# Kernel tuning notes

Measured on AMD Instinct MI355X. Metric: run time of the kernel, lower is better.

The kernel has to match this reference:

```python
import jax, jax.numpy as jnp
import numpy as np

DIM = 1024
S_SIZE = 512
M_SIZE = 4096
L_SIZE = 8192
MERGE_THRESHOLD = 0.98
L_ALPHA = 0.1
K_PROMOTE = max(1, S_SIZE // 4)  # torch: min(len(candidates), max(1, s_size//4)); candidates >> s_size here


def _l2norm(x, axis=-1):
    # F.normalize(p=2) with eps clamp
    return x / jnp.maximum(jnp.linalg.norm(x, axis=axis, keepdims=True), 1e-12)


def _update(processed_tokens, s_memory, m_memory, l_memory, m_utility, l_utility, wq, bq, wk, bk, s_ptr):
    cand = processed_tokens.reshape(-1, DIM)
    # --- S tier: scatter top-k-norm candidates into ring buffer (vectorized; K<=S so slots distinct) ---
    norms = jnp.linalg.norm(cand, axis=1)
    _, top_idx = jax.lax.top_k(norms, K_PROMOTE)
    pos = (s_ptr + jnp.arange(K_PROMOTE)) % S_SIZE
    s_mem = s_memory.at[pos].set(cand[top_idx])
    s_ptr_new = (s_ptr + K_PROMOTE) % S_SIZE
    # --- promotion attention (1 head, only attn weights used): pick best short-term slot ---
    q = l_memory.mean(axis=0) @ wq.T + bq                      # [dim]
    kproj = s_mem @ wk.T + bk                                  # [S, dim]
    attn = jax.nn.softmax(kproj @ q / jnp.sqrt(jnp.asarray(DIM, cand.dtype)))
    best_s_idx = jnp.argmax(attn)
    candidate = s_mem[best_s_idx]                              # [dim]

    # --- M tier: promote / merge / replace ---
    def not_full(mm, mu):
        ridx = jnp.argmin(mu)
        return mm.at[ridx].set(candidate), mu.at[ridx].set(mu.mean() + 1e-5)

    def full(mm, mu):
        mm_norm = _l2norm(mm)
        sims = mm_norm @ _l2norm(candidate)                    # [M]
        msi = jnp.argmax(sims)
        sim_cand = sims[msi]

        def merge_with_candidate(mm, mu):
            merged = _l2norm((mm[msi] + candidate) / 2.0)
            return mm.at[msi].set(merged), mu.at[msi].set((mu[msi] + mu.mean()) / 2.0)

        def try_internal_merge(mm, mu):
            # most redundant pair: strict lower triangle of cosine sim matrix
            sim_mat = mm_norm @ mm_norm.T                      # [M, M]
            sim_mat = jnp.where(jnp.triu(jnp.ones((M_SIZE, M_SIZE), bool)), -1.0, sim_mat)
            flat = jnp.argmax(sim_mat)
            internal_sim = sim_mat.reshape(-1)[flat]
            idx1, idx2 = flat // M_SIZE, flat % M_SIZE

            def do_pair_merge(mm, mu):
                merged = _l2norm((mm[idx1] + mm[idx2]) / 2.0)
                mm2 = mm.at[idx1].set(merged).at[idx2].set(candidate)
                mu1 = mu.at[idx1].set((mu[idx1] + mu[idx2]) / 2.0)
                mu2 = mu1.at[idx2].set(mu1.mean() + 1e-5)      # torch recomputes mean after idx1 write
                return mm2, mu2

            def replace_weakest(mm, mu):
                li = jnp.argmin(mu)
                stronger = jnp.linalg.norm(candidate) > jnp.linalg.norm(mm[li])
                mm2 = jnp.where(stronger, mm.at[li].set(candidate), mm)
                mu2 = jnp.where(stronger, mu.at[li].set(mu.mean() + 1e-5), mu)
                return mm2, mu2

            return jax.lax.cond(internal_sim > MERGE_THRESHOLD, do_pair_merge, replace_weakest, mm, mu)

        return jax.lax.cond(sim_cand > MERGE_THRESHOLD, merge_with_candidate, try_internal_merge, mm, mu)

    is_m_full = ~jnp.any(m_utility == 0)
    m_mem, m_util = jax.lax.cond(is_m_full, full, not_full, m_memory, m_utility)
    # --- L tier: consolidate most-used M slot into least-used L slot ---
    mi = jnp.argmax(m_util)
    lj = jnp.argmin(l_utility)
    consolidated = (1.0 - L_ALPHA) * l_memory[lj] + L_ALPHA * m_mem[mi]
    l_mem = l_memory.at[lj].set(consolidated)
    l_util = l_utility.at[lj].set(l_utility.mean())            # mean of pre-write values
    return s_mem, m_mem, l_mem, m_util, l_util, s_ptr_new


def setup_inputs() -> dict:
    key = jax.random.key(0)
    ks = jax.random.split(key, 10)
    scale = 1.0 / np.sqrt(DIM)
    return {
        "processed_tokens": jax.random.normal(ks[0], (4, 4096, DIM), jnp.float32),
        "s_memory": jax.random.normal(ks[1], (S_SIZE, DIM), jnp.float32),
        "m_memory": jax.random.normal(ks[2], (M_SIZE, DIM), jnp.float32),
        "l_memory": jax.random.normal(ks[3], (L_SIZE, DIM), jnp.float32),
        "m_utility": jax.random.uniform(ks[4], (M_SIZE,), jnp.float32) + 0.01,  # >0 -> 'm full' branch
        "l_utility": jax.random.uniform(ks[5], (L_SIZE,), jnp.float32) + 0.01,
        "wq": jax.random.normal(ks[6], (DIM, DIM), jnp.float32) * scale,
        "bq": jnp.zeros((DIM,), jnp.float32),
        "wk": jax.random.normal(ks[7], (DIM, DIM), jnp.float32) * scale,
        "bk": jnp.zeros((DIM,), jnp.float32),
        "s_ptr": 0,
    }


def reference(processed_tokens, s_memory, m_memory, l_memory, m_utility, l_utility, wq, bq, wk, bk, s_ptr):
    return _update(processed_tokens, s_memory, m_memory, l_memory, m_utility, l_utility, wq, bq, wk, bk, s_ptr)
```

## Files before the change

kernel.cpp:

```cpp
#include <hip/hip_runtime.h>

#define DIMV 1024
#define SSZ 512
#define MSZ 4096
#define LSZ 8192
#define KPROM 128
#define NCAND 16384
#define NPAIR 528

typedef __attribute__((ext_vector_type(4))) float f32x4;
typedef __attribute__((ext_vector_type(4))) unsigned int u32x4;
typedef __attribute__((ext_vector_type(4))) unsigned short u16x4;
typedef __attribute__((ext_vector_type(8))) __bf16 bf16x8;

#define OUT_S 0ull
#define OUT_M 524288ull
#define OUT_L 4718592ull
#define OUT_MU 13107200ull
#define OUT_LU 13111296ull
#define OUT_SPTR 13119488ull

#define SC_BF16 0ull
#define SC_NORMS 2100000ull
#define SC_TOPIDX 2117000ull
#define SC_LPART 2120000ull
#define SC_RV 2260000ull
#define SC_LMEAN 2262000ull
#define SC_LOGITS 2413000ull
#define SC_BEST 2414000ull
#define SC_MNORM 2415000ull
#define SC_SIMS 2420000ull
#define SC_PPV 2425000ull
#define SC_PPI 2427000ull

__device__ __forceinline__ float wave_sum(float v) {
#pragma unroll
  for (int o = 32; o > 0; o >>= 1) v += __shfl_down(v, o, 64);
  return v;
}
__device__ __forceinline__ void wave_maxidx(float& v, int& i) {
#pragma unroll
  for (int o = 32; o > 0; o >>= 1) {
    float ov = __shfl_down(v, o, 64);
    int oi = __shfl_down(i, o, 64);
    if (ov > v || (ov == v && oi < i)) { v = ov; i = oi; }
  }
}
__device__ __forceinline__ void wave_minidx(float& v, int& i) {
#pragma unroll
  for (int o = 32; o > 0; o >>= 1) {
    float ov = __shfl_down(v, o, 64);
    int oi = __shfl_down(i, o, 64);
    if (ov < v || (ov == v && oi < i)) { v = ov; i = oi; }
  }
}
__device__ __forceinline__ unsigned short f2bf(float x) {
  unsigned u = __float_as_uint(x);
  return (unsigned short)((u + 0x7FFFu + ((u >> 16) & 1u)) >> 16);
}
__device__ __forceinline__ void gload16(const unsigned short* g, unsigned short* l) {
  __builtin_amdgcn_global_load_lds((const __attribute__((address_space(1))) unsigned int*)(g),
                                   (__attribute__((address_space(3))) unsigned int*)(l), 16, 0, 0);
}

__global__ void kA(const float* __restrict__ cand, const float* __restrict__ l_memory,
                   const float* __restrict__ m, float* __restrict__ norms,
                   float* __restrict__ lpart, unsigned short* __restrict__ mb,
                   float* __restrict__ mnorm, float* __restrict__ rv) {
  int b = blockIdx.x, t = threadIdx.x, lane = t & 63, w = t >> 6;
  if (b < 128) {
    if (b == 0) {
      f32x4 z = {0.f, 0.f, 0.f, 0.f};
      ((f32x4*)rv)[t] = z;
    }
    f32x4 a0 = {0.f, 0.f, 0.f, 0.f}, a1 = a0, a2 = a0, a3 = a0;
    const f32x4* base = (const f32x4*)(l_memory + (size_t)b * 64 * DIMV);
#pragma unroll 4
    for (int r = 0; r < 64; r += 4) {
      a0 += base[(r + 0) * 256 + t];
      a1 += base[(r + 1) * 256 + t];
      a2 += base[(r + 2) * 256 + t];
      a3 += base[(r + 3) * 256 + t];
    }
    f32x4 a = (a0 + a1) + (a2 + a3);
    ((f32x4*)(lpart + (size_t)b * DIMV))[t] = a;
  } else if (b < 1152) {
    int r0 = (b - 128) * 16 + w * 4;
    const f32x4* base4 = (const f32x4*)(cand + (size_t)r0 * DIMV);
    float s0 = 0.f, s1 = 0.f, s2 = 0.f, s3 = 0.f;
#pragma unroll
    for (int k = 0; k < 16; ++k) {
      f32x4 v = base4[k * 64 + lane];
      float d = v.x * v.x + v.y * v.y + v.z * v.z + v.w * v.w;
      if (k < 4) s0 += d;
      else if (k < 8) s1 += d;
      else if (k < 12) s2 += d;
      else s3 += d;
    }
    f32x4 sv = {s0, s1, s2, s3};
#pragma unroll
    for (int o = 32; o > 0; o >>= 1) {
      sv.x += __shfl_down(sv.x, o, 64);
      sv.y += __shfl_down(sv.y, o, 64);
      sv.z += __shfl_down(sv.z, o, 64);
      sv.w += __shfl_down(sv.w, o, 64);
    }
    if (lane == 0) {
      f32x4 o4 = {sqrtf(sv.x), sqrtf(sv.y), sqrtf(sv.z), sqrtf(sv.w)};
      *((f32x4*)(norms + r0)) = o4;
    }
  } else {
    int r0 = (b - 1152) * 16 + w * 4;
    const f32x4* base4 = (const f32x4*)(m + (size_t)r0 * DIMV);
    u16x4* mb4 = (u16x4*)(mb + (size_t)r0 * DIMV);
    float s0 = 0.f, s1 = 0.f, s2 = 0.f, s3 = 0.f;
#pragma unroll
    for (int k = 0; k < 16; ++k) {
      int i = k * 64 + lane;
      f32x4 v = base4[i];
      float d = v.x * v.x + v.y * v.y + v.z * v.z + v.w * v.w;
      if (k < 4) s0 += d;
      else if (k < 8) s1 += d;
      else if (k < 12) s2 += d;
      else s3 += d;
      u16x4 h;
      h.x = f2bf(v.x); h.y = f2bf(v.y); h.z = f2bf(v.z); h.w = f2bf(v.w);
      mb4[i] = h;
    }
    f32x4 sv = {s0, s1, s2, s3};
#pragma unroll
    for (int o = 32; o > 0; o >>= 1) {
      sv.x += __shfl_down(sv.x, o, 64);
      sv.y += __shfl_down(sv.y, o, 64);
      sv.z += __shfl_down(sv.z, o, 64);
      sv.w += __shfl_down(sv.w, o, 64);
    }
    if (lane == 0) {
      f32x4 o4 = {sqrtf(sv.x), sqrtf(sv.y), sqrtf(sv.z), sqrtf(sv.w)};
      *((f32x4*)(mnorm + r0)) = o4;
    }
  }
}

__device__ int scan_excl_1024(int v, int* sh, int* total) {
  int t = threadIdx.x;
  sh[t] = v;
  __syncthreads();
  for (int o = 1; o < 1024; o <<= 1) {
    int x = (t >= o) ? sh[t - o] : 0;
    __syncthreads();
    sh[t] += x;
    __syncthreads();
  }
  int incl = sh[t];
  *total = sh[1023];
  __syncthreads();
  return incl - v;
}

__global__ void kT(const float* __restrict__ norms, int* __restrict__ topidx,
                   const float* __restrict__ lpart, float* __restrict__ lmean) {
  int t = threadIdx.x;
  if (blockIdx.x == 1) {
    float s0 = 0.f, s1 = 0.f, s2 = 0.f, s3 = 0.f;
    for (int p = 0; p < 128; p += 4) {
      s0 += lpart[(size_t)(p + 0) * DIMV + t];
      s1 += lpart[(size_t)(p + 1) * DIMV + t];
      s2 += lpart[(size_t)(p + 2) * DIMV + t];
      s3 += lpart[(size_t)(p + 3) * DIMV + t];
    }
    lmean[t] = ((s0 + s1) + (s2 + s3)) * (1.f / 8192.f);
    return;
  }
  int w = t >> 6;
  __shared__ int sh[1024];
  __shared__ int histW[16][256];
  __shared__ unsigned s_selkey[KPROM];
  __shared__ int s_selidx[KPROM];
  __shared__ int s_digit, s_sub;
  unsigned key[16];
#pragma unroll
  for (int j = 0; j < 16; ++j) key[j] = __float_as_uint(norms[t * 16 + j]);

  unsigned prefix = 0, himask = 0;
  int remaining = KPROM;
  for (int p = 24; p >= 0; p -= 8) {
#pragma unroll
    for (int i = 0; i < 4; ++i) ((int*)histW)[t + i * 1024] = 0;
    __syncthreads();
#pragma unroll
    for (int j = 0; j < 16; ++j)
      if ((key[j] & himask) == prefix) atomicAdd(&histW[w][(key[j] >> p) & 255], 1);
    __syncthreads();
    if (t < 256) {
      int h = 0;
#pragma unroll
      for (int w2 = 0; w2 < 16; ++w2) h += histW[w2][t];
      sh[t] = h;
    }
    __syncthreads();
    for (int o = 1; o < 256; o <<= 1) {
      int x = (t < 256 && t + o < 256) ? sh[t + o] : 0;
      __syncthreads();
      if (t < 256) sh[t] += x;
      __syncthreads();
    }
    if (t < 256) {
      int sfex = (t < 255) ? sh[t + 1] : 0;
      if (sfex < remaining && remaining <= sh[t]) { s_digit = t; s_sub = sfex; }
    }
    __syncthreads();
    prefix |= ((unsigned)s_digit) << p;
    remaining -= s_sub;
    himask |= (0xFFu << p);
    __syncthreads();
  }
  unsigned T = prefix;

  int cgt = 0, ceq = 0;
#pragma unroll
  for (int j = 0; j < 16; ++j) { cgt += (key[j] > T); ceq += (key[j] == T); }
  int total_gt, total_eq;
  int sgt = scan_excl_1024(cgt, sh, &total_gt);
  int seq = scan_excl_1024(ceq, sh, &total_eq);
  int need_eq = KPROM - total_gt;
  int g = sgt, e = seq;
#pragma unroll
  for (int j = 0; j < 16; ++j) {
    if (key[j] > T) { s_selkey[g] = key[j]; s_selidx[g] = t * 16 + j; ++g; }
    else if (key[j] == T) {
      if (e < need_eq) { s_selkey[total_gt + e] = key[j]; s_selidx[total_gt + e] = t * 16 + j; }
      ++e;
    }
  }
  __syncthreads();
  if (t < KPROM) {
    unsigned mk = s_selkey[t];
    int mi = s_selidx[t];
    int rank = 0;
    for (int q2 = 0; q2 < KPROM; ++q2) {
      unsigned qk = s_selkey[q2];
      int qi = s_selidx[q2];
      rank += (qk > mk || (qk == mk && qi < mi)) ? 1 : 0;
    }
    topidx[rank] = mi;
  }
}

__global__ void kBC(const float* __restrict__ cand, const float* __restrict__ s_memory,
                    const int* __restrict__ topidx, const int* __restrict__ s_ptr,
                    const float* __restrict__ wq, const float* __restrict__ bq,
                    const float* __restrict__ wk, const float* __restrict__ lmean,
                    float* __restrict__ out_s, float* __restrict__ out_sptr,
                    float* __restrict__ rv) {
  int b = blockIdx.x, t = threadIdx.x, lane = t & 63, w = t >> 6;
  if (b < 512) {
    int sp = s_ptr[0];
    int k = (b - sp + SSZ) & (SSZ - 1);
    const float* src = (k < KPROM) ? (cand + (size_t)topidx[k] * DIMV) : (s_memory + (size_t)b * DIMV);
    ((f32x4*)(out_s + (size_t)b * DIMV))[t] = ((const f32x4*)src)[t];
    if (b == 0 && t == 0) out_sptr[0] = (float)((sp + KPROM) % SSZ);
    return;
  }
  __shared__ float qs[8];
  int qb = b - 512;
  const f32x4* lm = (const f32x4*)lmean;
#pragma unroll
  for (int rr = 0; rr < 2; ++rr) {
    int d = qb * 8 + w * 2 + rr;
    const f32x4* row = (const f32x4*)(wq + (size_t)d * DIMV);
    float s = 0.f;
#pragma unroll
    for (int c = 0; c < 4; ++c) {
      f32x4 a = row[c * 64 + lane], bb = lm[c * 64 + lane];
      s += a.x * bb.x + a.y * bb.y + a.z * bb.z + a.w * bb.w;
    }
    s = wave_sum(s);
    if (lane == 0) qs[w * 2 + rr] = s + bq[d];
  }
  __syncthreads();
  f32x4 a = {0.f, 0.f, 0.f, 0.f};
#pragma unroll
  for (int r = 0; r < 8; ++r) {
    float qd = qs[r];
    f32x4 v = ((const f32x4*)(wk + (size_t)(qb * 8 + r) * DIMV))[t];
    a += v * qd;
  }
  atomicAdd(&rv[t * 4 + 0], a.x);
  atomicAdd(&rv[t * 4 + 1], a.y);
  atomicAdd(&rv[t * 4 + 2], a.z);
  atomicAdd(&rv[t * 4 + 3], a.w);
}

__global__ void kD(const float* __restrict__ out_s, const float* __restrict__ rv,
                   float* __restrict__ logits) {
  int lane = threadIdx.x & 63, w = threadIdx.x >> 6;
  int srow = blockIdx.x * 4 + w;
  const f32x4* a = (const f32x4*)(out_s + (size_t)srow * DIMV);
  const f32x4* b = (const f32x4*)rv;
  float s = 0.f;
#pragma unroll
  for (int c = 0; c < 4; ++c) {
    f32x4 x = a[c * 64 + lane], y = b[c * 64 + lane];
    s += x.x * y.x + x.y * y.y + x.z * y.z + x.w * y.w;
  }
  s = wave_sum(s);
  if (lane == 0) logits[srow] = s;
}

__global__ void kE(const float* __restrict__ logits, const float* __restrict__ out_s,
                   int* __restrict__ best, float* __restrict__ cnorm) {
  __shared__ float swv[4];
  __shared__ int swi[4];
  int t = threadIdx.x, lane = t & 63, w = t >> 6;
  float v0 = logits[t], v1 = logits[t + 256];
  float bv;
  int bidx;
  if (v1 > v0) { bv = v1; bidx = t + 256; } else { bv = v0; bidx = t; }
  wave_maxidx(bv, bidx);
  if (lane == 0) { swv[w] = bv; swi[w] = bidx; }
  __syncthreads();
  if (t == 0) {
    float a = swv[0]; int ai = swi[0];
    for (int i = 1; i < 4; ++i)
      if (swv[i] > a || (swv[i] == a && swi[i] < ai)) { a = swv[i]; ai = swi[i]; }
    best[0] = ai;
  }
  __syncthreads();
  int bi = best[0];
  f32x4 c4 = ((const f32x4*)(out_s + (size_t)bi * DIMV))[t];
  float s = c4.x * c4.x + c4.y * c4.y + c4.z * c4.z + c4.w * c4.w;
  s = wave_sum(s);
  __syncthreads();
  if (lane == 0) swv[w] = s;
  __syncthreads();
  if (t == 0) cnorm[0] = sqrtf(swv[0] + swv[1] + swv[2] + swv[3]);
}

__global__ __launch_bounds__(256, 3) void kG(const unsigned short* __restrict__ mb,
                                             const float* __restrict__ mnorm,
                                             const float* __restrict__ m,
                                             const float* __restrict__ out_s,
                                             const int* __restrict__ best,
                                             const float* __restrict__ cnorm,
                                             float* __restrict__ pv, int* __restrict__ pidx,
                                             float* __restrict__ sims) {
  int b = blockIdx.x, t = threadIdx.x, lane = t & 63, w = t >> 6;
  if (b >= NPAIR) {
    int row = (b - NPAIR) * 4 + w;
    const f32x4* mp = (const f32x4*)(m + (size_t)row * DIMV);
    const f32x4* cp = (const f32x4*)(out_s + (size_t)best[0] * DIMV);
    float sd = 0.f;
#pragma unroll
    for (int c = 0; c < 4; ++c) {
      int i = c * 64 + lane;
      f32x4 v = mp[i], u = cp[i];
      sd += v.x * u.x + v.y * u.y + v.z * u.z + v.w * u.w;
    }
    sd = wave_sum(sd);
    if (lane == 0) sims[row] = sd / (fmaxf(mnorm[row], 1e-12f) * fmaxf(cnorm[0], 1e-12f));
    return;
  }
  __shared__ unsigned short Ash[128 * 64];
  __shared__ unsigned short Bsh[128 * 64];
  __shared__ float spv[4];
  __shared__ int spi[4];

  int bs = (b & 7) * 66 + (b >> 3);
  int bi = (int)((sqrtf(8.f * (float)bs + 1.f) - 1.f) * 0.5f);
  while (bi * (bi + 1) / 2 > bs) --bi;
  while ((bi + 1) * (bi + 2) / 2 <= bs) ++bi;
  int bj = bs - bi * (bi + 1) / 2;
  int rowA0 = bi * 128, rowB0 = bj * 128;

  int wr = w >> 1, wc = w & 1;
  int rl = lane & 15, kq4 = lane >> 4;
  int swz = rl & 7;
  int subrow = lane >> 3, gg = lane & 7;
  int gsw = (gg ^ subrow) << 3;

  f32x4 acc[4][4];
  f32x4 z = {0.f, 0.f, 0.f, 0.f};
#pragma unroll
  for (int ti = 0; ti < 4; ++ti)
#pragma unroll
    for (int tj = 0; tj < 4; ++tj) acc[ti][tj] = z;

  for (int kc = 0; kc < DIMV; kc += 64) {
#pragma unroll
    for (int jj = 0; jj < 4; ++jj) {
      int rsub = w * 32 + jj * 8 + subrow;
      gload16(mb + (size_t)(rowA0 + rsub) * DIMV + kc + gsw, Ash + (w * 4 + jj) * 512);
      gload16(mb + (size_t)(rowB0 + rsub) * DIMV + kc + gsw, Bsh + (w * 4 + jj) * 512);
    }
    __syncthreads();
#pragma unroll
    for (int ks = 0; ks < 2; ++ks) {
      int co = (((ks * 4 + kq4) ^ swz) << 3);
      bf16x8 af[4], bfv[4];
#pragma unroll
      for (int ti = 0; ti < 4; ++ti)
        af[ti] = *(const bf16x8*)(Ash + (wr * 64 + ti * 16 + rl) * 64 + co);
#pragma unroll
      for (int tj = 0; tj < 4; ++tj)
        bfv[tj] = *(const bf16x8*)(Bsh + (wc * 64 + tj * 16 + rl) * 64 + co);
#pragma unroll
      for (int ti = 0; ti < 4; ++ti)
#pragma unroll
        for (int tj = 0; tj < 4; ++tj)
          acc[ti][tj] = __builtin_amdgcn_mfma_f32_16x16x32_bf16(af[ti], bfv[tj], acc[ti][tj], 0, 0, 0);
    }
    __syncthreads();
  }

  float ni[16], nj4[4];
#pragma unroll
  for (int ti = 0; ti < 4; ++ti)
#pragma unroll
    for (int r = 0; r < 4; ++r)
      ni[ti * 4 + r] = fmaxf(mnorm[rowA0 + wr * 64 + ti * 16 + kq4 * 4 + r], 1e-12f);
#pragma unroll
  for (int tj = 0; tj < 4; ++tj)
    nj4[tj] = fmaxf(mnorm[rowB0 + wc * 64 + tj * 16 + rl], 1e-12f);

  float bv = -3.402823466e38f;
  int bidx = 0x7FFFFFFF;
#pragma unroll
  for (int ti = 0; ti < 4; ++ti)
#pragma unroll
    for (int tj = 0; tj < 4; ++tj)
#pragma unroll
      for (int r = 0; r < 4; ++r) {
        int gi = rowA0 + wr * 64 + ti * 16 + kq4 * 4 + r;
        int gj = rowB0 + wc * 64 + tj * 16 + rl;
        if (gi > gj) {
          float s = acc[ti][tj][r] / (ni[ti * 4 + r] * nj4[tj]);
          int fi = gi * MSZ + gj;
          if (s > bv || (s == bv && fi < bidx)) { bv = s; bidx = fi; }
        }
      }
  wave_maxidx(bv, bidx);
  if (lane == 0) { spv[w] = bv; spi[w] = bidx; }
  __syncthreads();
  if (t == 0) {
    float a = spv[0]; int ai = spi[0];
    for (int i = 1; i < 4; ++i)
      if (spv[i] > a || (spv[i] == a && spi[i] < ai)) { a = spv[i]; ai = spi[i]; }
    pv[b] = a;
    pidx[b] = ai;
  }
}

__global__ void kH(const float* __restrict__ pv, const int* __restrict__ pidx,
                   const float* __restrict__ sims, const float* __restrict__ mu,
                   const float* __restrict__ mnorm, const float* __restrict__ cnorm,
                   const int* __restrict__ best, const float* __restrict__ lu,
                   float* __restrict__ out_mu, float* __restrict__ out_lu,
                   int* __restrict__ ws) {
  __shared__ float swv[16];
  __shared__ int swi[16];
  __shared__ float ssum[16];
  __shared__ int szf[16];
  __shared__ float s_res[2];
  __shared__ int s_resi[2];
  __shared__ int s_branch, s_i1, s_i2, s_lj;
  __shared__ float s_u1, s_u2, s_lmean;
  int t = threadIdx.x, lane = t & 63, w = t >> 6;

  float bv = -3.402823466e38f;
  int bidx = 0x7FFFFFFF;
  for (int i = t; i < NPAIR; i += 1024) {
    float v = pv[i];
    int fi = pidx[i];
    if (v > bv || (v == bv && fi < bidx)) { bv = v; bidx = fi; }
  }
  wave_maxidx(bv, bidx);
  if (lane == 0) { swv[w] = bv; swi[w] = bidx; }
  __syncthreads();
  if (t == 0) {
    float a = swv[0]; int ai = swi[0];
    for (int i = 1; i < 16; ++i)
      if (swv[i] > a || (swv[i] == a && swi[i] < ai)) { a = swv[i]; ai = swi[i]; }
    s_res[0] = a; s_resi[0] = ai;
  }
  __syncthreads();

  bv = -3.402823466e38f;
  bidx = 0x7FFFFFFF;
#pragma unroll
  for (int j = 0; j < 4; ++j) {
    int i = t * 4 + j;
    float v = sims[i];
    if (v > bv) { bv = v; bidx = i; }
  }
  wave_maxidx(bv, bidx);
  if (lane == 0) { swv[w] = bv; swi[w] = bidx; }
  __syncthreads();
  if (t == 0) {
    float a = swv[0]; int ai = swi[0];
    for (int i = 1; i < 16; ++i)
      if (swv[i] > a || (swv[i] == a && swi[i] < ai)) { a = swv[i]; ai = swi[i]; }
    s_res[1] = a; s_resi[1] = ai;
  }
  __syncthreads();

  float muv[4];
  float sum = 0.f, mnv = 3.402823466e38f;
  int mni = 0x7FFFFFFF, zf = 0;
#pragma unroll
  for (int j = 0; j < 4; ++j) {
    int i = t * 4 + j;
    float v = mu[i];
    muv[j] = v;
    sum += v;
    if (v < mnv) { mnv = v; mni = i; }
    if (v == 0.f) zf = 1;
  }
  sum = wave_sum(sum);
  wave_minidx(mnv, mni);
#pragma unroll
  for (int o = 32; o > 0; o >>= 1) zf |= __shfl_down(zf, o, 64);
  if (lane == 0) { ssum[w] = sum; swv[w] = mnv; swi[w] = mni; szf[w] = zf; }
  __syncthreads();
  if (t == 0) {
    float muSum = 0.f;
    int anyz = 0;
    float a = swv[0]; int li = swi[0];
    for (int i = 0; i < 16; ++i) {
      muSum += ssum[i];
      anyz |= szf[i];
      if (i > 0 && (swv[i] < a || (swv[i] == a && swi[i] < li))) { a = swv[i]; li = swi[i]; }
    }
    float muMean = muSum / 4096.f;
    float internal_sim = s_res[0];
    int iflat = s_resi[0];
    float sim_cand = s_res[1];
    int msi = s_resi[1];
    int branch, i1 = -1, i2 = -1;
    float u1 = 0.f, u2 = 0.f;
    if (anyz) {
      branch = 0; i1 = li; u1 = muMean + 1e-5f;
    } else if (sim_cand > 0.98f) {
      branch = 1; i1 = msi; u1 = (mu[msi] + muMean) * 0.5f;
    } else if (internal_sim > 0.98f) {
      branch = 2; i1 = iflat / MSZ; i2 = iflat - (iflat / MSZ) * MSZ;
      float o1 = mu[i1], o2 = mu[i2];
      u1 = (o1 + o2) * 0.5f;
      u2 = (muSum - o1 + u1) / 4096.f + 1e-5f;
    } else {
      if (cnorm[0] > mnorm[li]) { branch = 0; i1 = li; u1 = muMean + 1e-5f; }
      else branch = 4;
    }
    s_branch = branch; s_i1 = i1; s_i2 = i2; s_u1 = u1; s_u2 = u2;
    ws[2] = branch; ws[3] = i1; ws[4] = i2; ws[5] = best[0];
  }
  __syncthreads();

  int branch = s_branch, i1 = s_i1, i2 = s_i2;
  float u1 = s_u1, u2 = s_u2;
  bv = -3.402823466e38f;
  bidx = 0x7FFFFFFF;
#pragma unroll
  for (int j = 0; j < 4; ++j) {
    int i = t * 4 + j;
    float v = muv[j];
    if (branch != 4 && i == i1) v = u1;
    if (branch == 2 && i == i2) v = u2;
    out_mu[i] = v;
    if (v > bv) { bv = v; bidx = i; }
  }
  wave_maxidx(bv, bidx);
  __syncthreads();
  if (lane == 0) { swv[w] = bv; swi[w] = bidx; }
  __syncthreads();
  if (t == 0) {
    float a = swv[0]; int ai = swi[0];
    for (int i = 1; i < 16; ++i)
      if (swv[i] > a || (swv[i] == a && swi[i] < ai)) { a = swv[i]; ai = swi[i]; }
    ws[1] = ai;
  }

  float luv[8];
  sum = 0.f; mnv = 3.402823466e38f; mni = 0x7FFFFFFF;
#pragma unroll
  for (int j = 0; j < 8; ++j) {
    int i = t * 8 + j;
    float v = lu[i];
    luv[j] = v;
    sum += v;
    if (v < mnv) { mnv = v; mni = i; }
  }
  sum = wave_sum(sum);
  wave_minidx(mnv, mni);
  __syncthreads();
  if (lane == 0) { swv[w] = mnv; swi[w] = mni; ssum[w] = sum; }
  __syncthreads();
  if (t == 0) {
    float a = swv[0]; int ai = swi[0];
    float ls = 0.f;
    for (int i = 0; i < 16; ++i) {
      ls += ssum[i];
      if (i > 0 && (swv[i] < a || (swv[i] == a && swi[i] < ai))) { a = swv[i]; ai = swi[i]; }
    }
    s_lj = ai;
    s_lmean = ls / 8192.f;
    ws[0] = ai;
  }
  __syncthreads();
  int lj = s_lj;
  float lmv = s_lmean;
#pragma unroll
  for (int j = 0; j < 8; ++j) {
    int i = t * 8 + j;
    out_lu[i] = (i == lj) ? lmv : luv[j];
  }
}

__global__ void kI(const float* __restrict__ m, const float* __restrict__ l_memory,
                   const float* __restrict__ out_s, const int* __restrict__ ws,
                   float* __restrict__ out_m, float* __restrict__ out_l) {
  __shared__ float sred[4];
  int b = blockIdx.x, t = threadIdx.x, lane = t & 63, w = t >> 6;
  int lj = ws[0], mi = ws[1], branch = ws[2], i1 = ws[3], i2 = ws[4], best = ws[5];
  if (b < 1024) {
    int r0 = b * 4;
    bool special = (branch != 4) &&
                   ((i1 >= r0 && i1 < r0 + 4) || (branch == 2 && i2 >= r0 && i2 < r0 + 4));
    if (!special) {
      const f32x4* src = (const f32x4*)(m + (size_t)r0 * DIMV);
      f32x4* dst = (f32x4*)(out_m + (size_t)r0 * DIMV);
#pragma unroll
      for (int k = 0; k < 4; ++k) dst[k * 256 + t] = src[k * 256 + t];
      return;
    }
    for (int rr = 0; rr < 4; ++rr) {
      int row = r0 + rr;
      int mode = 0;
      if ((branch == 0 && row == i1) || (branch == 2 && row == i2)) mode = 1;
      else if (branch == 1 && row == i1) mode = 2;
      else if (branch == 2 && row == i1) mode = 3;
      f32x4* dst = (f32x4*)(out_m + (size_t)row * DIMV);
      if (mode == 0) {
        dst[t] = ((const f32x4*)(m + (size_t)row * DIMV))[t];
      } else if (mode == 1) {
        dst[t] = ((const f32x4*)(out_s + (size_t)best * DIMV))[t];
      } else {
        f32x4 a = ((const f32x4*)(m + (size_t)row * DIMV))[t];
        f32x4 bb = (mode == 2) ? ((const f32x4*)(out_s + (size_t)best * DIMV))[t]
                               : ((const f32x4*)(m + (size_t)i2 * DIMV))[t];
        f32x4 v = (a + bb) * 0.5f;
        float ss = v.x * v.x + v.y * v.y + v.z * v.z + v.w * v.w;
        ss = wave_sum(ss);
        if (lane == 0) sred[w] = ss;
        __syncthreads();
        float nrm = fmaxf(sqrtf(sred[0] + sred[1] + sred[2] + sred[3]), 1e-12f);
        __syncthreads();
        dst[t] = v / nrm;
      }
    }
  } else {
    int r0 = (b - 1024) * 4;
    bool special = (lj >= r0 && lj < r0 + 4);
    if (!special) {
      const f32x4* src = (const f32x4*)(l_memory + (size_t)r0 * DIMV);
      f32x4* dst = (f32x4*)(out_l + (size_t)r0 * DIMV);
#pragma unroll
      for (int k = 0; k < 4; ++k) dst[k * 256 + t] = src[k * 256 + t];
      return;
    }
    for (int rr = 0; rr < 4; ++rr) {
      int row = r0 + rr;
      f32x4 v = ((const f32x4*)(l_memory + (size_t)row * DIMV))[t];
      if (row == lj) {
        int mode = 0;
        if ((branch == 0 && mi == i1) || (branch == 2 && mi == i2)) mode = 1;
        else if (branch == 1 && mi == i1) mode = 2;
        else if (branch == 2 && mi == i1) mode = 3;
        f32x4 mv;
        if (mode == 0) {
          mv = ((const f32x4*)(m + (size_t)mi * DIMV))[t];
        } else if (mode == 1) {
          mv = ((const f32x4*)(out_s + (size_t)best * DIMV))[t];
        } else {
          f32x4 a = ((const f32x4*)(m + (size_t)mi * DIMV))[t];
          f32x4 bb = (mode == 2) ? ((const f32x4*)(out_s + (size_t)best * DIMV))[t]
                                 : ((const f32x4*)(m + (size_t)i2 * DIMV))[t];
          f32x4 vm = (a + bb) * 0.5f;
          float ss = vm.x * vm.x + vm.y * vm.y + vm.z * vm.z + vm.w * vm.w;
          ss = wave_sum(ss);
          if (lane == 0) sred[w] = ss;
          __syncthreads();
          float nrm = fmaxf(sqrtf(sred[0] + sred[1] + sred[2] + sred[3]), 1e-12f);
          __syncthreads();
          mv = vm / nrm;
        }
        v = v * 0.9f + mv * 0.1f;
      }
      ((f32x4*)(out_l + (size_t)row * DIMV))[t] = v;
    }
  }
}

extern "C" void kernel_launch(void* const* d_in, const int* in_sizes, int n_in,
                              void* d_out, int out_size, void* d_ws, size_t ws_size,
                              hipStream_t stream) {
  const float* cand = (const float*)d_in[0];
  const float* s_memory = (const float*)d_in[1];
  const float* m_memory = (const float*)d_in[2];
  const float* l_memory = (const float*)d_in[3];
  const float* m_utility = (const float*)d_in[4];
  const float* l_utility = (const float*)d_in[5];
  const float* wq = (const float*)d_in[6];
  const float* bq = (const float*)d_in[7];
  const float* wk = (const float*)d_in[8];
  const float* bk = (const float*)d_in[9];
  const int* s_ptr = (const int*)d_in[10];
  (void)bk;

  float* out = (float*)d_out;
  float* out_s = out + OUT_S;
  float* out_m = out + OUT_M;
  float* out_l = out + OUT_L;
  float* out_mu = out + OUT_MU;
  float* out_lu = out + OUT_LU;
  float* out_sptr = out + OUT_SPTR;

  float* lsc = out_l;
  unsigned short* mb = (unsigned short*)(lsc + SC_BF16);
  float* norms = lsc + SC_NORMS;
  int* topidx = (int*)(lsc + SC_TOPIDX);
  float* lpart = lsc + SC_LPART;
  float* rv = lsc + SC_RV;
  float* lmean = lsc + SC_LMEAN;
  float* logits = lsc + SC_LOGITS;
  int* best = (int*)(lsc + SC_BEST);
  float* cnorm = lsc + SC_BEST + 1;
  float* mnorm = lsc + SC_MNORM;
  float* sims = lsc + SC_SIMS;
  float* pv = lsc + SC_PPV;
  int* pidx = (int*)(lsc + SC_PPI);
  int* wsctl = (int*)d_ws;

  kA<<<1408, 256, 0, stream>>>(cand, l_memory, m_memory, norms, lpart, mb, mnorm, rv);
  kT<<<2, 1024, 0, stream>>>(norms, topidx, lpart, lmean);
  kBC<<<640, 256, 0, stream>>>(cand, s_memory, topidx, s_ptr, wq, bq, wk, lmean, out_s, out_sptr,
                               rv);
  kD<<<128, 256, 0, stream>>>(out_s, rv, logits);
  kE<<<1, 256, 0, stream>>>(logits, out_s, best, cnorm);
  kG<<<NPAIR + 1024, 256, 0, stream>>>(mb, mnorm, m_memory, out_s, best, cnorm, pv, pidx, sims);
  kH<<<1, 1024, 0, stream>>>(pv, pidx, sims, m_utility, mnorm, cnorm, best, l_utility,
                             out_mu, out_lu, wsctl);
  kI<<<3072, 256, 0, stream>>>(m_memory, l_memory, out_s, wsctl, out_m, out_l);
}
```

Measured before the change: 277.6 us.

## Fuse argmax kernel into logits kernel via packed atomicMax and recompute candidate norm

Removes the single-block kE launch. kD now reduces each block's logits to a packed 64-bit key (order-preserving float bits plus inverted row index) and combines blocks with a global atomicMax. The candidate norm is recomputed redundantly in kG blocks and in kH. The change also packs the two top-k scans in kT into one and pads the histogram rows to avoid LDS bank conflicts. It saves one launch and one serialized tiny kernel at the cost of some duplicated norm work.

Result: no change. 279.4 us (+0.7%).

```diff
diff --git a/kernel.cpp b/kernel.cpp
--- a/kernel.cpp
+++ b/kernel.cpp
@@ -26,8 +26,7 @@
 #define SC_LPART 2120000ull
 #define SC_RV 2260000ull
 #define SC_LMEAN 2262000ull
-#define SC_LOGITS 2413000ull
-#define SC_BEST 2414000ull
+#define SC_BPK 2414000ull
 #define SC_MNORM 2415000ull
 #define SC_SIMS 2420000ull
 #define SC_PPV 2425000ull
@@ -66,12 +65,14 @@
 __global__ void kA(const float* __restrict__ cand, const float* __restrict__ l_memory,
                    const float* __restrict__ m, float* __restrict__ norms,
                    float* __restrict__ lpart, unsigned short* __restrict__ mb,
-                   float* __restrict__ mnorm, float* __restrict__ rv) {
+                   float* __restrict__ mnorm, float* __restrict__ rv,
+                   unsigned long long* __restrict__ bestPack) {
   int b = blockIdx.x, t = threadIdx.x, lane = t & 63, w = t >> 6;
   if (b < 128) {
     if (b == 0) {
       f32x4 z = {0.f, 0.f, 0.f, 0.f};
       ((f32x4*)rv)[t] = z;
+      if (t == 0) bestPack[0] = 0ull;
     }
     f32x4 a0 = {0.f, 0.f, 0.f, 0.f}, a1 = a0, a2 = a0, a3 = a0;
     const f32x4* base = (const f32x4*)(l_memory + (size_t)b * 64 * DIMV);
@@ -174,7 +175,7 @@
   }
   int w = t >> 6;
   __shared__ int sh[1024];
-  __shared__ int histW[16][256];
+  __shared__ int histW[16][257];
   __shared__ unsigned s_selkey[KPROM];
   __shared__ int s_selidx[KPROM];
   __shared__ int s_digit, s_sub;
@@ -185,8 +186,7 @@
   unsigned prefix = 0, himask = 0;
   int remaining = KPROM;
   for (int p = 24; p >= 0; p -= 8) {
-#pragma unroll
-    for (int i = 0; i < 4; ++i) ((int*)histW)[t + i * 1024] = 0;
+    for (int i = t; i < 16 * 257; i += 1024) ((int*)histW)[i] = 0;
     __syncthreads();
 #pragma unroll
     for (int j = 0; j < 16; ++j)
@@ -220,9 +220,10 @@
   int cgt = 0, ceq = 0;
 #pragma unroll
   for (int j = 0; j < 16; ++j) { cgt += (key[j] > T); ceq += (key[j] == T); }
-  int total_gt, total_eq;
-  int sgt = scan_excl_1024(cgt, sh, &total_gt);
-  int seq = scan_excl_1024(ceq, sh, &total_eq);
+  int total_pk;
+  int spk = scan_excl_1024((cgt << 15) | ceq, sh, &total_pk);
+  int sgt = spk >> 15, seq = spk & 0x7FFF;
+  int total_gt = total_pk >> 15;
   int need_eq = KPROM - total_gt;
   int g = sgt, e = seq;
 #pragma unroll
@@ -293,8 +294,9 @@
 }
 
 __global__ void kD(const float* __restrict__ out_s, const float* __restrict__ rv,
-                   float* __restrict__ logits) {
-  int lane = threadIdx.x & 63, w = threadIdx.x >> 6;
+                   unsigned long long* __restrict__ bestPack) {
+  __shared__ unsigned long long spk[4];
+  int t = threadIdx.x, lane = t & 63, w = t >> 6;
   int srow = blockIdx.x * 4 + w;
   const f32x4* a = (const f32x4*)(out_s + (size_t)srow * DIMV);
   const f32x4* b = (const f32x4*)rv;
@@ -305,60 +307,45 @@
     s += x.x * y.x + x.y * y.y + x.z * y.z + x.w * y.w;
   }
   s = wave_sum(s);
-  if (lane == 0) logits[srow] = s;
-}
-
-__global__ void kE(const float* __restrict__ logits, const float* __restrict__ out_s,
-                   int* __restrict__ best, float* __restrict__ cnorm) {
-  __shared__ float swv[4];
-  __shared__ int swi[4];
-  int t = threadIdx.x, lane = t & 63, w = t >> 6;
-  float v0 = logits[t], v1 = logits[t + 256];
-  float bv;
-  int bidx;
-  if (v1 > v0) { bv = v1; bidx = t + 256; } else { bv = v0; bidx = t; }
-  wave_maxidx(bv, bidx);
-  if (lane == 0) { swv[w] = bv; swi[w] = bidx; }
+  if (lane == 0) {
+    unsigned u = __float_as_uint(s);
+    u = (u & 0x80000000u) ? ~u : (u | 0x80000000u);
+    spk[w] = ((unsigned long long)u << 32) | (unsigned)(~srow);
+  }
   __syncthreads();
   if (t == 0) {
-    float a = swv[0]; int ai = swi[0];
+    unsigned long long m0 = spk[0];
     for (int i = 1; i < 4; ++i)
-      if (swv[i] > a || (swv[i] == a && swi[i] < ai)) { a = swv[i]; ai = swi[i]; }
-    best[0] = ai;
-  }
-  __syncthreads();
-  int bi = best[0];
-  f32x4 c4 = ((const f32x4*)(out_s + (size_t)bi * DIMV))[t];
-  float s = c4.x * c4.x + c4.y * c4.y + c4.z * c4.z + c4.w * c4.w;
-  s = wave_sum(s);
-  __syncthreads();
-  if (lane == 0) swv[w] = s;
-  __syncthreads();
-  if (t == 0) cnorm[0] = sqrtf(swv[0] + swv[1] + swv[2] + swv[3]);
+      if (spk[i] > m0) m0 = spk[i];
+    atomicMax(bestPack, m0);
+  }
 }
 
 __global__ __launch_bounds__(256, 3) void kG(const unsigned short* __restrict__ mb,
                                              const float* __restrict__ mnorm,
                                              const float* __restrict__ m,
                                              const float* __restrict__ out_s,
-                                             const int* __restrict__ best,
-                                             const float* __restrict__ cnorm,
+                                             const unsigned long long* __restrict__ bestPack,
                                              float* __restrict__ pv, int* __restrict__ pidx,
                                              float* __restrict__ sims) {
   int b = blockIdx.x, t = threadIdx.x, lane = t & 63, w = t >> 6;
   if (b >= NPAIR) {
     int row = (b - NPAIR) * 4 + w;
+    int bi = ~((unsigned)(bestPack[0] & 0xFFFFFFFFull));
     const f32x4* mp = (const f32x4*)(m + (size_t)row * DIMV);
-    const f32x4* cp = (const f32x4*)(out_s + (size_t)best[0] * DIMV);
-    float sd = 0.f;
+    const f32x4* cp = (const f32x4*)(out_s + (size_t)bi * DIMV);
+    float sd = 0.f, cd = 0.f;
 #pragma unroll
     for (int c = 0; c < 4; ++c) {
       int i = c * 64 + lane;
       f32x4 v = mp[i], u = cp[i];
       sd += v.x * u.x + v.y * u.y + v.z * u.z + v.w * u.w;
+      cd += u.x * u.x + u.y * u.y + u.z * u.z + u.w * u.w;
     }
     sd = wave_sum(sd);
-    if (lane == 0) sims[row] = sd / (fmaxf(mnorm[row], 1e-12f) * fmaxf(cnorm[0], 1e-12f));
+    cd = wave_sum(cd);
+    if (lane == 0)
+      sims[row] = sd / (fmaxf(mnorm[row], 1e-12f) * fmaxf(sqrtf(cd), 1e-12f));
     return;
   }
   __shared__ unsigned short Ash[128 * 64];
@@ -453,8 +440,9 @@
 
 __global__ void kH(const float* __restrict__ pv, const int* __restrict__ pidx,
                    const float* __restrict__ sims, const float* __restrict__ mu,
-                   const float* __restrict__ mnorm, const float* __restrict__ cnorm,
-                   const int* __restrict__ best, const float* __restrict__ lu,
+                   const float* __restrict__ mnorm,
+                   const unsigned long long* __restrict__ bestPack,
+                   const float* __restrict__ lu, const float* __restrict__ out_s,
                    float* __restrict__ out_mu, float* __restrict__ out_lu,
                    int* __restrict__ ws) {
   __shared__ float swv[16];
@@ -463,9 +451,28 @@
   __shared__ int szf[16];
   __shared__ float s_res[2];
   __shared__ int s_resi[2];
-  __shared__ int s_branch, s_i1, s_i2, s_lj;
-  __shared__ float s_u1, s_u2, s_lmean;
+  __shared__ int s_branch, s_i1, s_i2, s_lj, s_bi;
+  __shared__ float s_u1, s_u2, s_lmean, s_cn;
   int t = threadIdx.x, lane = t & 63, w = t >> 6;
+
+  if (t == 0) s_bi = ~((unsigned)(bestPack[0] & 0xFFFFFFFFull));
+  __syncthreads();
+  {
+    float cs = 0.f;
+    if (t < 256) {
+      f32x4 c4 = ((const f32x4*)(out_s + (size_t)s_bi * DIMV))[t];
+      cs = c4.x * c4.x + c4.y * c4.y + c4.z * c4.z + c4.w * c4.w;
+    }
+    cs = wave_sum(cs);
+    if (lane == 0) ssum[w] = cs;
+    __syncthreads();
+    if (t == 0) {
+      float s2 = 0.f;
+      for (int i = 0; i < 16; ++i) s2 += ssum[i];
+      s_cn = sqrtf(s2);
+    }
+    __syncthreads();
+  }
 
   float bv = -3.402823466e38f;
   int bidx = 0x7FFFFFFF;
@@ -548,11 +555,11 @@
       u1 = (o1 + o2) * 0.5f;
       u2 = (muSum - o1 + u1) / 4096.f + 1e-5f;
     } else {
-      if (cnorm[0] > mnorm[li]) { branch = 0; i1 = li; u1 = muMean + 1e-5f; }
+      if (s_cn > mnorm[li]) { branch = 0; i1 = li; u1 = muMean + 1e-5f; }
       else branch = 4;
     }
     s_branch = branch; s_i1 = i1; s_i2 = i2; s_u1 = u1; s_u2 = u2;
-    ws[2] = branch; ws[3] = i1; ws[4] = i2; ws[5] = best[0];
+    ws[2] = branch; ws[3] = i1; ws[4] = i2; ws[5] = s_bi;
   }
   __syncthreads();
 
@@ -732,23 +739,20 @@
   float* lpart = lsc + SC_LPART;
   float* rv = lsc + SC_RV;
   float* lmean = lsc + SC_LMEAN;
-  float* logits = lsc + SC_LOGITS;
-  int* best = (int*)(lsc + SC_BEST);
-  float* cnorm = lsc + SC_BEST + 1;
+  unsigned long long* bestPack = (unsigned long long*)(lsc + SC_BPK);
   float* mnorm = lsc + SC_MNORM;
   float* sims = lsc + SC_SIMS;
   float* pv = lsc + SC_PPV;
   int* pidx = (int*)(lsc + SC_PPI);
   int* wsctl = (int*)d_ws;
 
-  kA<<<1408, 256, 0, stream>>>(cand, l_memory, m_memory, norms, lpart, mb, mnorm, rv);
+  kA<<<1408, 256, 0, stream>>>(cand, l_memory, m_memory, norms, lpart, mb, mnorm, rv, bestPack);
   kT<<<2, 1024, 0, stream>>>(norms, topidx, lpart, lmean);
   kBC<<<640, 256, 0, stream>>>(cand, s_memory, topidx, s_ptr, wq, bq, wk, lmean, out_s, out_sptr,
                                rv);
-  kD<<<128, 256, 0, stream>>>(out_s, rv, logits);
-  kE<<<1, 256, 0, stream>>>(logits, out_s, best, cnorm);
-  kG<<<NPAIR + 1024, 256, 0, stream>>>(mb, mnorm, m_memory, out_s, best, cnorm, pv, pidx, sims);
-  kH<<<1, 1024, 0, stream>>>(pv, pidx, sims, m_utility, mnorm, cnorm, best, l_utility,
+  kD<<<128, 256, 0, stream>>>(out_s, rv, bestPack);
+  kG<<<NPAIR + 1024, 256, 0, stream>>>(mb, mnorm, m_memory, out_s, bestPack, pv, pidx, sims);
+  kH<<<1, 1024, 0, stream>>>(pv, pidx, sims, m_utility, mnorm, bestPack, l_utility, out_s,
                              out_mu, out_lu, wsctl);
   kI<<<3072, 256, 0, stream>>>(m_memory, l_memory, out_s, wsctl, out_m, out_l);
 }
```
